# Kernel tuning notes

Hardware: AMD Instinct MI355X
Metric: run time of the kernel (lower is better)

The kernel has to match this reference:

```python
import jax, jax.numpy as jnp
import numpy as np

# config constants (init_kwargs)
WC, WS = 0.5, 0.5            # boundary cosine / structural weights (hybrid mode)
TARGET_BPP = 6.0             # target_bytes_per_patch
GAIN = 1.0                   # target_patch_gain
THRESH = 0.5                 # boundary_threshold; mask = p >= THRESH
EPS = 1e-6

_POP6 = jnp.array([bin(i).count('1') for i in range(64)], dtype=jnp.int32)

def _pop6(x):
    return _POP6[jnp.clip(x, 0, 63)]

def _logit(p):
    p = jnp.clip(p, EPS, 1.0 - EPS)
    return jnp.log(p) - jnp.log1p(-p)

def _next(x):  # shift-left by one, zero-padded at end (matches torch q_next pattern)
    return jnp.concatenate([x[1:], jnp.zeros((1,), x.dtype)])

def _hist(vals, mask, bins):
    idx = jnp.where(mask, vals, bins)  # invalid -> out of range, dropped
    return jnp.zeros((bins,), jnp.int32).at[idx].add(1, mode='drop')


def setup_inputs() -> dict:
    key = jax.random.key(0)
    ks = jax.random.split(key, 6)
    B, S = 4, 1048576
    return {
        'boundary_logprobs': jax.random.normal(ks[0], (B, S), jnp.float32),
        'states': jax.random.randint(ks[1], (B, S), 0, 4096, jnp.int32),
        'q_class': jax.random.randint(ks[2], (B, S), 0, 64, jnp.int32),
        'family': jax.random.randint(ks[3], (B, S), 0, 4, jnp.int32),
        'micro_ref': jax.random.randint(ks[4], (B, S), 0, 64, jnp.int32),
        'valid_mask': jax.random.randint(ks[5], (B, S), 0, 2, jnp.int32).astype(bool),
    }


def reference(boundary_logprobs, states, q_class, family, micro_ref, valid_mask):
    B, S = valid_mask.shape
    v = valid_mask.reshape(-1)
    st = states.reshape(-1).astype(jnp.int32)
    q = q_class.reshape(-1).astype(jnp.int32)
    fam = family.reshape(-1).astype(jnp.int32)
    mic = micro_ref.reshape(-1).astype(jnp.int32)

    # --- structural boundary probs ---
    omega12 = st & 0xFFF
    c6 = ((omega12 >> 6) ^ omega12) & 63          # chirality6
    d_chi = jnp.clip(_pop6(c6 ^ _next(c6)).astype(jnp.float32) / 6.0, 0.0, 1.0)
    d_q = _pop6((q & 63) ^ (_next(q) & 63)).astype(jnp.float32) / 6.0
    fx = (fam & 3) ^ (_next(fam) & 3)
    d_fam = (((fx & 1) != 0).astype(jnp.float32) + ((fx & 2) != 0).astype(jnp.float32)) / 2.0
    score = jnp.clip(0.5 * d_chi + 0.35 * d_q + 0.15 * d_fam, EPS, 1.0)
    structural = jnp.where(v, score, 0.0)

    # --- combine with cosine probs (hybrid mode) ---
    cosine = jnp.exp(jnp.minimum(boundary_logprobs.reshape(-1), 0.0))
    combined = (WC * cosine + WS * structural) / max(WC + WS, 1e-6)

    # --- target bytes-per-patch rate adjustment ---
    vf = v.astype(jnp.float32)
    vc = jnp.maximum(jnp.sum(vf), 1.0)
    cur = jnp.clip(jnp.sum(combined * vf) / vc, 1e-4, 1.0 - 1e-4)
    tgt = max(1e-4, min(1.0 - 1e-4, 1.0 / TARGET_BPP))
    shift = _logit(jnp.asarray(tgt, jnp.float32)) - _logit(cur)
    combined = jax.nn.sigmoid(_logit(combined) + GAIN * shift)
    combined = jnp.clip(combined, EPS, 1.0 - EPS)
    combined_logprobs = jnp.log(combined)
    bmask = combined_logprobs >= jnp.log(jnp.asarray(THRESH, jnp.float32))

    # --- histograms over effective (valid) positions ---
    shell = _pop6(c6)
    q_hist64 = _hist(q, v, 64)
    family_hist4 = _hist(fam, v, 4)
    micro_hist64 = _hist(mic, v, 64)
    shell_hist7 = _hist(shell, v, 7)
    wt_q = _pop6(q & 63)
    q_weight_hist7 = _hist(wt_q, v, 7)
    bits = ((q & 63)[:, None] >> jnp.arange(6)) & 1            # [n, 6]
    bit_excitation6 = jnp.sum(bits * v[:, None].astype(jnp.int32), axis=0)

    # --- patch lengths (vectorized run-length over valid bytes) ---
    bv = bmask & v
    pos = jnp.cumsum(v.astype(jnp.int32))                      # 1-indexed valid position
    bpos = jnp.where(bv, pos, 0)
    prev = jax.lax.cummax(jnp.concatenate([jnp.zeros((1,), jnp.int32), bpos[:-1]]))
    lengths = jnp.where(bv, pos - prev, 0)                     # dense run lengths at boundaries
    total_valid = pos[-1]
    trailing = total_valid - jax.lax.cummax(bpos)[-1]          # open trailing run
    patch_count = jnp.sum(bv).astype(jnp.int32) + (trailing > 0).astype(jnp.int32)

    return (combined_logprobs.reshape(B, S), bmask.reshape(B, S), structural.reshape(B, S),
            q_hist64, family_hist4, micro_hist64, shell_hist7, q_weight_hist7,
            bit_excitation6, lengths, trailing, patch_count)
```

## Files before the change

### kernel.cpp

```cpp
#include <hip/hip_runtime.h>

#define TPB 256
#define EPT 8
#define CHUNK (TPB * EPT)
#define P2T 1024
#define NSLICE 64

typedef unsigned long long ull;
typedef long long ll;

__device__ __forceinline__ ull shfl_down_u64(ull x, int off) {
    unsigned lo = (unsigned)x, hi = (unsigned)(x >> 32);
    lo = __shfl_down(lo, off, 64);
    hi = __shfl_down(hi, off, 64);
    return ((ull)hi << 32) | lo;
}

__global__ __launch_bounds__(TPB, 8) void k_pass1(
    const float* __restrict__ blp, const int* __restrict__ st,
    const int* __restrict__ q, const int* __restrict__ fam,
    const int* __restrict__ mic, const int* __restrict__ vm,
    float* __restrict__ out_structural,
    int* __restrict__ ghist, ull* __restrict__ l1sum, int n)
{
    __shared__ int lh2[2048];
    __shared__ int slhs[11];
    __shared__ int swv[4];
    __shared__ float swc[4];

    const int tid = threadIdx.x, lane = tid & 63, wave = tid >> 6;
    const long i0 = (long)blockIdx.x * CHUNK + (long)tid * EPT;
    const bool fast = ((long)(blockIdx.x + 1) * CHUNK <= n);

    int stv[9], qv[9], fv[9], micv[8], vmv[8];
    float bpv[8];
    if (fast) {
        const int4 sa = *(const int4*)(st + i0),  sb = *(const int4*)(st + i0 + 4);
        const int4 qa = *(const int4*)(q + i0),   qb = *(const int4*)(q + i0 + 4);
        const int4 fa = *(const int4*)(fam + i0), fb = *(const int4*)(fam + i0 + 4);
        const int4 ma = *(const int4*)(mic + i0), mb = *(const int4*)(mic + i0 + 4);
        const int4 va = *(const int4*)(vm + i0),  vb = *(const int4*)(vm + i0 + 4);
        const float4 ba = *(const float4*)(blp + i0), bb = *(const float4*)(blp + i0 + 4);
        int nst = __shfl_down(sa.x, 1, 64);
        int nq  = __shfl_down(qa.x, 1, 64);
        int nf  = __shfl_down(fa.x, 1, 64);
        if (lane == 63) {
            const long j = i0 + 8;
            nst = (j < n) ? st[j]  : 0;
            nq  = (j < n) ? q[j]   : 0;
            nf  = (j < n) ? fam[j] : 0;
        }
        stv[0]=sa.x; stv[1]=sa.y; stv[2]=sa.z; stv[3]=sa.w; stv[4]=sb.x; stv[5]=sb.y; stv[6]=sb.z; stv[7]=sb.w; stv[8]=nst;
        qv[0]=qa.x;  qv[1]=qa.y;  qv[2]=qa.z;  qv[3]=qa.w;  qv[4]=qb.x;  qv[5]=qb.y;  qv[6]=qb.z;  qv[7]=qb.w;  qv[8]=nq;
        fv[0]=fa.x;  fv[1]=fa.y;  fv[2]=fa.z;  fv[3]=fa.w;  fv[4]=fb.x;  fv[5]=fb.y;  fv[6]=fb.z;  fv[7]=fb.w;  fv[8]=nf;
        micv[0]=ma.x; micv[1]=ma.y; micv[2]=ma.z; micv[3]=ma.w; micv[4]=mb.x; micv[5]=mb.y; micv[6]=mb.z; micv[7]=mb.w;
        vmv[0]=va.x; vmv[1]=va.y; vmv[2]=va.z; vmv[3]=va.w; vmv[4]=vb.x; vmv[5]=vb.y; vmv[6]=vb.z; vmv[7]=vb.w;
        bpv[0]=ba.x; bpv[1]=ba.y; bpv[2]=ba.z; bpv[3]=ba.w; bpv[4]=bb.x; bpv[5]=bb.y; bpv[6]=bb.z; bpv[7]=bb.w;
    } else {
        #pragma unroll
        for (int e = 0; e < 8; ++e) {
            long ii = i0 + e;
            bool r = ii < n;
            stv[e] = r ? st[ii] : 0;  qv[e] = r ? q[ii] : 0;  fv[e] = r ? fam[ii] : 0;
            micv[e] = r ? mic[ii] : 0; vmv[e] = r ? vm[ii] : 0; bpv[e] = r ? blp[ii] : 0.f;
        }
        stv[8] = (i0 + 8 < n) ? st[i0 + 8] : 0;
        qv[8]  = (i0 + 8 < n) ? q[i0 + 8] : 0;
        fv[8]  = (i0 + 8 < n) ? fam[i0 + 8] : 0;
    }

    {
        int4 z4; z4.x = 0; z4.y = 0; z4.z = 0; z4.w = 0;
        *(int4*)&lh2[tid * 8] = z4;
        *(int4*)&lh2[tid * 8 + 4] = z4;
    }
    if (tid < 11) slhs[tid] = 0;
    __syncthreads();

    const int qrow = ((wave << 2) | (lane & 3)) << 6;
    int sv = 0;
    float scf = 0.0f;
    ull accF = 0, accS0 = 0, accS1 = 0;
    float structural[8];
    #pragma unroll
    for (int e = 0; e < 8; ++e) {
        int sti = stv[e], qi = qv[e], fi = fv[e], mi = micv[e];
        int v = (vmv[e] != 0);
        int om  = sti & 0xFFF;      int c6  = ((om  >> 6) ^ om ) & 63;
        int omn = stv[e+1] & 0xFFF; int c6n = ((omn >> 6) ^ omn) & 63;
        float d_chi = (float)__popc(c6 ^ c6n) * (1.0f / 6.0f);
        float d_q   = (float)__popc((qi & 63) ^ (qv[e+1] & 63)) * (1.0f / 6.0f);
        int fx = (fi & 3) ^ (fv[e+1] & 3);
        float d_fam = (float)((fx & 1) + ((fx >> 1) & 1)) * 0.5f;
        float score = 0.5f * d_chi + 0.35f * d_q + 0.15f * d_fam;
        score = fminf(fmaxf(score, 1e-6f), 1.0f);
        structural[e] = v ? score : 0.0f;
        float cosine = expf(fminf(bpv[e], 0.0f));
        float combined = 0.5f * (cosine + structural[e]);
        if (v) {
            sv += 1;
            scf += combined;
            atomicAdd(&lh2[qrow + (qi & 63)], 1);
            atomicAdd(&lh2[1024 + qrow + (mi & 63)], 1);
            accF += 1ULL << ((fi & 3) * 16);
            int sh = __popc(c6);
            ull ts = 1ULL << ((sh & 3) * 16);
            if (sh < 4) accS0 += ts; else accS1 += ts;
        }
    }

    if (fast) {
        float4 o;
        o.x=structural[0]; o.y=structural[1]; o.z=structural[2]; o.w=structural[3];
        *(float4*)(out_structural + i0) = o;
        o.x=structural[4]; o.y=structural[5]; o.z=structural[6]; o.w=structural[7];
        *(float4*)(out_structural + i0 + 4) = o;
    } else {
        #pragma unroll
        for (int e = 0; e < 8; ++e)
            if (i0 + e < n) out_structural[i0 + e] = structural[e];
    }

    #pragma unroll
    for (int off = 32; off > 0; off >>= 1) {
        sv  += __shfl_down(sv, off, 64);
        scf += __shfl_down(scf, off, 64);
        accF  += shfl_down_u64(accF, off);
        accS0 += shfl_down_u64(accS0, off);
        accS1 += shfl_down_u64(accS1, off);
    }
    if (lane == 0) {
        swv[wave] = sv; swc[wave] = scf;
        #pragma unroll
        for (int b2 = 0; b2 < 4; ++b2) atomicAdd(&slhs[b2],     (int)((accF  >> (16*b2)) & 0xFFFF));
        #pragma unroll
        for (int b2 = 0; b2 < 4; ++b2) atomicAdd(&slhs[4 + b2], (int)((accS0 >> (16*b2)) & 0xFFFF));
        #pragma unroll
        for (int b2 = 0; b2 < 3; ++b2) atomicAdd(&slhs[8 + b2], (int)((accS1 >> (16*b2)) & 0xFFFF));
    }
    __syncthreads();
    if (tid == 0) {
        int vsum = swv[0] + swv[1] + swv[2] + swv[3];
        double cs = (double)swc[0] + (double)swc[1] + (double)swc[2] + (double)swc[3];
        ll cf = (ll)(cs * 16384.0 + 0.5);
        atomicAdd(&l1sum[blockIdx.x >> 5], ((ull)(unsigned)vsum << 39) | (ull)cf);
    }
    if (tid < 139) {
        const int t2 = tid;
        int val;
        if (t2 < 64) {
            val = 0;
            #pragma unroll
            for (int r = 0; r < 16; ++r) val += lh2[(r << 6) + t2];
        } else if (t2 < 68) {
            val = slhs[t2 - 64];
        } else if (t2 < 132) {
            int b2 = t2 - 68;
            val = 0;
            #pragma unroll
            for (int r = 0; r < 16; ++r) val += lh2[1024 + (r << 6) + b2];
        } else {
            val = slhs[4 + (t2 - 132)];
        }
        if (val) atomicAdd(&ghist[(blockIdx.x & (NSLICE - 1)) * 152 + t2], val);
    }
}

__global__ __launch_bounds__(TPB, 8) void k_pass3(
    const float* __restrict__ strc, const float* __restrict__ blp,
    const ull* __restrict__ l1sum, const int* __restrict__ ghist,
    float* __restrict__ out_logp, float* __restrict__ out_bmask,
    float* __restrict__ out_len, int* __restrict__ chunk_cnt,
    int* __restrict__ chunk_lastloc, ull* __restrict__ chunk_first,
    int* __restrict__ chunk_vsum, float* __restrict__ out_hist, int n)
{
    __shared__ int swt[4], swm[4], scnt[4];
    __shared__ float sShift;
    __shared__ int qh[64];
    const int tid = threadIdx.x, lane = tid & 63, wave = tid >> 6;
    const long i0 = (long)blockIdx.x * CHUNK + (long)tid * EPT;
    const bool fast = ((long)(blockIdx.x + 1) * CHUNK <= n);
    const int nb = (int)gridDim.x;

    float sv8[8], bp8[8];
    if (fast) {
        const float4 s0 = *(const float4*)(strc + i0), s1 = *(const float4*)(strc + i0 + 4);
        const float4 p0 = *(const float4*)(blp + i0),  p1 = *(const float4*)(blp + i0 + 4);
        sv8[0]=s0.x; sv8[1]=s0.y; sv8[2]=s0.z; sv8[3]=s0.w; sv8[4]=s1.x; sv8[5]=s1.y; sv8[6]=s1.z; sv8[7]=s1.w;
        bp8[0]=p0.x; bp8[1]=p0.y; bp8[2]=p0.z; bp8[3]=p0.w; bp8[4]=p1.x; bp8[5]=p1.y; bp8[6]=p1.z; bp8[7]=p1.w;
    } else {
        #pragma unroll
        for (int e = 0; e < 8; ++e) {
            long ii = i0 + e;
            bool r = ii < n;
            sv8[e] = r ? strc[ii] : 0.0f;
            bp8[e] = r ? blp[ii] : 0.0f;
        }
    }

    if (wave == 0) {
        const int ngrp = (nb + 31) >> 5;
        int vt = 0; ll ct = 0;
        for (int gg = lane; gg < ngrp; gg += 64) {
            ull cell = l1sum[gg];
            vt += (int)(cell >> 39);
            ct += (ll)(cell & ((1ULL << 39) - 1));
        }
        #pragma unroll
        for (int off = 32; off > 0; off >>= 1) {
            vt += __shfl_down(vt, off, 64);
            ct += (ll)shfl_down_u64((ull)ct, off);
        }
        if (lane == 0) {
            double vcd = (double)(vt > 1 ? vt : 1);
            float cur = (float)(((double)ct * (1.0 / 16384.0)) / vcd);
            cur = fminf(fmaxf(cur, 1e-4f), 0.9999f);
            float p = fminf(fmaxf(cur, 1e-6f), 0.999999f);
            float lc = logf(p) - log1pf(-p);
            float tgt = (float)(1.0 / 6.0);
            float lt = logf(tgt) - log1pf(-tgt);
            sShift = lt - lc;
        }
    }
    __syncthreads();
    const float K = expf(-sShift);

    unsigned mv = 0, mb = 0;
    float lp[8], bmf[8], lenv[8];
    #pragma unroll
    for (int e = 0; e < 8; ++e) {
        float s = sv8[e];
        int v = (s > 0.0f);
        float cosine = expf(fminf(bp8[e], 0.0f));
        float comb = 0.5f * (cosine + s);
        float p = fminf(fmaxf(comb, 1e-6f), 0.999999f);
        float d = fmaf(K, 1.0f - p, p);
        float sgm = p / d;
        sgm = fminf(fmaxf(sgm, 1e-6f), 0.999999f);
        float clp = logf(sgm);
        lp[e] = clp;
        int bm = (clp >= -0.69314718f) ? 1 : 0;
        bmf[e] = (float)bm;
        mv |= (unsigned)v << e;
        if (bm & v) mb |= 1u << e;
        lenv[e] = 0.0f;
    }
    if (fast) {
        float4 o;
        o.x=lp[0]; o.y=lp[1]; o.z=lp[2]; o.w=lp[3];     *(float4*)(out_logp + i0) = o;
        o.x=lp[4]; o.y=lp[5]; o.z=lp[6]; o.w=lp[7];     *(float4*)(out_logp + i0 + 4) = o;
        o.x=bmf[0]; o.y=bmf[1]; o.z=bmf[2]; o.w=bmf[3]; *(float4*)(out_bmask + i0) = o;
        o.x=bmf[4]; o.y=bmf[5]; o.z=bmf[6]; o.w=bmf[7]; *(float4*)(out_bmask + i0 + 4) = o;
    } else {
        #pragma unroll
        for (int e = 0; e < 8; ++e)
            if (i0 + e < n) { out_logp[i0 + e] = lp[e]; out_bmask[i0 + e] = bmf[e]; }
    }

    int tvc = __popc(mv);
    int x = tvc;
    #pragma unroll
    for (int off = 1; off < 64; off <<= 1) {
        int y = __shfl_up(x, off, 64);
        if (lane >= off) x += y;
    }
    if (lane == 63) swt[wave] = x;
    __syncthreads();
    int wb = 0;
    for (int w2 = 0; w2 < wave; ++w2) wb += swt[w2];
    const int vbase = wb + (x - tvc);

    int last = -1;
    if (mb) {
        int hb = 31 - __clz(mb);
        last = vbase + __popc(mv & ((2u << hb) - 1));
    }
    int m = last;
    #pragma unroll
    for (int off = 1; off < 64; off <<= 1) {
        int y = __shfl_up(m, off, 64);
        if (lane >= off && y > m) m = y;
    }
    int exm = __shfl_up(m, 1, 64);
    if (lane == 0) exm = -1;
    if (lane == 63) swm[wave] = m;
    int cnt = __popc(mb);
    ull fp = ~0ULL;
    if (mb) {
        int lb = __ffs(mb) - 1;
        int fv2 = vbase + __popc(mv & ((2u << lb) - 1));
        fp = ((ull)(unsigned)(i0 + lb) << 32) | (unsigned)fv2;
    }
    #pragma unroll
    for (int off = 32; off > 0; off >>= 1) {
        cnt += __shfl_down(cnt, off, 64);
        ull fo = shfl_down_u64(fp, off);
        if (fo < fp) fp = fo;
    }
    __shared__ ull sfirst[4];
    if (lane == 0) { scnt[wave] = cnt; sfirst[wave] = fp; }
    __syncthreads();

    int prev = exm;
    for (int w2 = 0; w2 < wave; ++w2) if (swm[w2] > prev) prev = swm[w2];
    int runv = 0;
    #pragma unroll
    for (int e = 0; e < 8; ++e) {
        runv += (mv >> e) & 1;
        if ((mb >> e) & 1) {
            int pos = vbase + runv;
            lenv[e] = (prev >= 0) ? (float)(pos - prev) : 0.0f;
            prev = pos;
        }
    }
    if (fast) {
        float4 o;
        o.x=lenv[0]; o.y=lenv[1]; o.z=lenv[2]; o.w=lenv[3]; *(float4*)(out_len + i0) = o;
        o.x=lenv[4]; o.y=lenv[5]; o.z=lenv[6]; o.w=lenv[7]; *(float4*)(out_len + i0 + 4) = o;
    } else {
        #pragma unroll
        for (int e = 0; e < 8; ++e)
            if (i0 + e < n) out_len[i0 + e] = lenv[e];
    }
    if (tid == 0) {
        int c = scnt[0] + scnt[1] + scnt[2] + scnt[3];
        int L = swm[0];
        if (swm[1] > L) L = swm[1];
        if (swm[2] > L) L = swm[2];
        if (swm[3] > L) L = swm[3];
        ull F = sfirst[0];
        if (sfirst[1] < F) F = sfirst[1];
        if (sfirst[2] < F) F = sfirst[2];
        if (sfirst[3] < F) F = sfirst[3];
        chunk_cnt[blockIdx.x] = c;
        chunk_lastloc[blockIdx.x] = L > 0 ? L : 0;
        chunk_first[blockIdx.x] = F;
        chunk_vsum[blockIdx.x] = swt[0] + swt[1] + swt[2] + swt[3];
    }

    if (blockIdx.x == 0) {
        if (tid < 139) {
            int acc = 0;
            #pragma unroll 8
            for (int sl = 0; sl < NSLICE; ++sl) acc += ghist[sl * 152 + tid];
            out_hist[tid] = (float)acc;
            if (tid < 64) qh[tid] = acc;
        }
        __syncthreads();
        if (tid < 7) {
            int sacc = 0;
            for (int b = 0; b < 64; ++b) if (__popc(b) == tid) sacc += qh[b];
            out_hist[139 + tid] = (float)sacc;
        }
        if (tid < 6) {
            int sacc = 0;
            for (int b = 0; b < 64; ++b) sacc += qh[b] * ((b >> tid) & 1);
            out_hist[146 + tid] = (float)sacc;
        }
    }
}

__global__ __launch_bounds__(P2T) void k_pass4(
    const int* __restrict__ chunk_cnt, const int* __restrict__ chunk_lastloc,
    const ull* __restrict__ chunk_first, const int* __restrict__ chunk_vsum,
    int nb, float* __restrict__ out_len,
    float* __restrict__ out_trailing, float* __restrict__ out_patch)
{
    __shared__ int ss[P2T];
    __shared__ int sm[P2T];
    __shared__ int sc[P2T];
    int t = threadIdx.x;
    int c0 = 2 * t, c1 = 2 * t + 1;
    int v0 = (c0 < nb) ? chunk_vsum[c0] : 0;
    int v1 = (c1 < nb) ? chunk_vsum[c1] : 0;
    int l0 = (c0 < nb) ? chunk_lastloc[c0] : 0;
    int l1 = (c1 < nb) ? chunk_lastloc[c1] : 0;
    int k0 = (c0 < nb) ? chunk_cnt[c0] : 0;
    int k1 = (c1 < nb) ? chunk_cnt[c1] : 0;
    ss[t] = v0 + v1;
    sc[t] = k0 + k1;
    __syncthreads();
    for (int off = 1; off < P2T; off <<= 1) {
        int add = (t >= off) ? ss[t - off] : 0;
        __syncthreads();
        ss[t] += add;
        __syncthreads();
    }
    const int vbase0 = ss[t] - v0 - v1;
    const int vbase1 = ss[t] - v1;
    const int total_v = ss[P2T - 1];
    const int gl0 = (l0 > 0) ? vbase0 + l0 : 0;
    const int gl1 = (l1 > 0) ? vbase1 + l1 : 0;
    sm[t] = gl0 > gl1 ? gl0 : gl1;
    __syncthreads();
    for (int off = 1; off < P2T; off <<= 1) {
        int y = (t >= off) ? sm[t - off] : 0;
        __syncthreads();
        if (y > sm[t]) sm[t] = y;
        __syncthreads();
    }
    const int excl = (t > 0) ? sm[t - 1] : 0;
    if (c0 < nb) {
        ull F = chunk_first[c0];
        if (F != ~0ULL) {
            int fi = (int)(F >> 32);
            int fv = (int)(F & 0xFFFFFFFFu);
            out_len[fi] = (float)(vbase0 + fv - excl);
        }
    }
    const int carry1 = excl > gl0 ? excl : gl0;
    if (c1 < nb) {
        ull F = chunk_first[c1];
        if (F != ~0ULL) {
            int fi = (int)(F >> 32);
            int fv = (int)(F & 0xFFFFFFFFu);
            out_len[fi] = (float)(vbase1 + fv - carry1);
        }
    }
    const int gmax = sm[P2T - 1];
    __syncthreads();
    for (int off = P2T / 2; off > 0; off >>= 1) {
        if (t < off) sc[t] += sc[t + off];
        __syncthreads();
    }
    if (t == 0) {
        int trailing = total_v - gmax;
        *out_trailing = (float)trailing;
        *out_patch = (float)(sc[0] + (trailing > 0 ? 1 : 0));
    }
}

extern "C" void kernel_launch(void* const* d_in, const int* in_sizes, int n_in,
                              void* d_out, int out_size, void* d_ws, size_t ws_size,
                              hipStream_t stream)
{
    const float* blp = (const float*)d_in[0];
    const int* st   = (const int*)d_in[1];
    const int* q    = (const int*)d_in[2];
    const int* fam  = (const int*)d_in[3];
    const int* mic  = (const int*)d_in[4];
    const int* vm   = (const int*)d_in[5];
    const int n = in_sizes[0];
    const int nb = (n + CHUNK - 1) / CHUNK;

    float* out = (float*)d_out;
    float* out_logp       = out;
    float* out_bmask      = out + (size_t)n;
    float* out_structural = out + 2 * (size_t)n;
    float* out_hist       = out + 3 * (size_t)n;
    float* out_len        = out + 3 * (size_t)n + 152;
    float* out_trailing   = out + 4 * (size_t)n + 152;
    float* out_patch      = out + 4 * (size_t)n + 153;

    char* w = (char*)d_ws;
    int*  ghist         = (int*)(w);
    ull*  l1sum         = (ull*)(w + 38912);
    int*  chunk_cnt     = (int*)(w + 40960);
    int*  chunk_lastloc = (int*)(w + 49152);
    int*  chunk_vsum    = (int*)(w + 57344);
    ull*  chunk_first   = (ull*)(w + 65536);

    hipMemsetAsync(w, 0, 39424, stream);

    k_pass1<<<dim3(nb), dim3(TPB), 0, stream>>>(
        blp, st, q, fam, mic, vm, out_structural, ghist, l1sum, n);

    k_pass3<<<dim3(nb), dim3(TPB), 0, stream>>>(
        out_structural, blp, l1sum, ghist,
        out_logp, out_bmask, out_len, chunk_cnt, chunk_lastloc, chunk_first,
        chunk_vsum, out_hist, n);

    k_pass4<<<dim3(1), dim3(P2T), 0, stream>>>(
        chunk_cnt, chunk_lastloc, chunk_first, chunk_vsum, nb, out_len,
        out_trailing, out_patch);
}
```

Measured before the change: 173.4 us.

## Halve elements per thread and scan four chunks per thread in pass4

Cuts elements per thread from 8 to 4, doubling the block count of pass1 and pass3 to raise parallelism and spread the per-block atomics and reductions. With N=4M this gives 4096 chunks, so the single-block pass4 scan now has each thread handle four chunks serially. The workspace offsets and memset size grow to fit the larger per-chunk arrays. The trade-off is more blocks doing block-level setup, more global histogram atomics, and a longer serial section in pass4.

```diff
diff --git a/kernel.cpp b/kernel.cpp
--- a/kernel.cpp
+++ b/kernel.cpp
@@ -1,7 +1,7 @@
 #include <hip/hip_runtime.h>
 
 #define TPB 256
-#define EPT 8
+#define EPT 4
 #define CHUNK (TPB * EPT)
 #define P2T 1024
 #define NSLICE 64
@@ -32,41 +32,41 @@
     const long i0 = (long)blockIdx.x * CHUNK + (long)tid * EPT;
     const bool fast = ((long)(blockIdx.x + 1) * CHUNK <= n);
 
-    int stv[9], qv[9], fv[9], micv[8], vmv[8];
-    float bpv[8];
+    int stv[5], qv[5], fv[5], micv[4], vmv[4];
+    float bpv[4];
     if (fast) {
-        const int4 sa = *(const int4*)(st + i0),  sb = *(const int4*)(st + i0 + 4);
-        const int4 qa = *(const int4*)(q + i0),   qb = *(const int4*)(q + i0 + 4);
-        const int4 fa = *(const int4*)(fam + i0), fb = *(const int4*)(fam + i0 + 4);
-        const int4 ma = *(const int4*)(mic + i0), mb = *(const int4*)(mic + i0 + 4);
-        const int4 va = *(const int4*)(vm + i0),  vb = *(const int4*)(vm + i0 + 4);
-        const float4 ba = *(const float4*)(blp + i0), bb = *(const float4*)(blp + i0 + 4);
+        const int4 sa = *(const int4*)(st + i0);
+        const int4 qa = *(const int4*)(q + i0);
+        const int4 fa = *(const int4*)(fam + i0);
+        const int4 ma = *(const int4*)(mic + i0);
+        const int4 va = *(const int4*)(vm + i0);
+        const float4 ba = *(const float4*)(blp + i0);
         int nst = __shfl_down(sa.x, 1, 64);
         int nq  = __shfl_down(qa.x, 1, 64);
         int nf  = __shfl_down(fa.x, 1, 64);
         if (lane == 63) {
-            const long j = i0 + 8;
+            const long j = i0 + 4;
             nst = (j < n) ? st[j]  : 0;
             nq  = (j < n) ? q[j]   : 0;
             nf  = (j < n) ? fam[j] : 0;
         }
-        stv[0]=sa.x; stv[1]=sa.y; stv[2]=sa.z; stv[3]=sa.w; stv[4]=sb.x; stv[5]=sb.y; stv[6]=sb.z; stv[7]=sb.w; stv[8]=nst;
-        qv[0]=qa.x;  qv[1]=qa.y;  qv[2]=qa.z;  qv[3]=qa.w;  qv[4]=qb.x;  qv[5]=qb.y;  qv[6]=qb.z;  qv[7]=qb.w;  qv[8]=nq;
-        fv[0]=fa.x;  fv[1]=fa.y;  fv[2]=fa.z;  fv[3]=fa.w;  fv[4]=fb.x;  fv[5]=fb.y;  fv[6]=fb.z;  fv[7]=fb.w;  fv[8]=nf;
-        micv[0]=ma.x; micv[1]=ma.y; micv[2]=ma.z; micv[3]=ma.w; micv[4]=mb.x; micv[5]=mb.y; micv[6]=mb.z; micv[7]=mb.w;
-        vmv[0]=va.x; vmv[1]=va.y; vmv[2]=va.z; vmv[3]=va.w; vmv[4]=vb.x; vmv[5]=vb.y; vmv[6]=vb.z; vmv[7]=vb.w;
-        bpv[0]=ba.x; bpv[1]=ba.y; bpv[2]=ba.z; bpv[3]=ba.w; bpv[4]=bb.x; bpv[5]=bb.y; bpv[6]=bb.z; bpv[7]=bb.w;
+        stv[0]=sa.x; stv[1]=sa.y; stv[2]=sa.z; stv[3]=sa.w; stv[4]=nst;
+        qv[0]=qa.x;  qv[1]=qa.y;  qv[2]=qa.z;  qv[3]=qa.w;  qv[4]=nq;
+        fv[0]=fa.x;  fv[1]=fa.y;  fv[2]=fa.z;  fv[3]=fa.w;  fv[4]=nf;
+        micv[0]=ma.x; micv[1]=ma.y; micv[2]=ma.z; micv[3]=ma.w;
+        vmv[0]=va.x; vmv[1]=va.y; vmv[2]=va.z; vmv[3]=va.w;
+        bpv[0]=ba.x; bpv[1]=ba.y; bpv[2]=ba.z; bpv[3]=ba.w;
     } else {
         #pragma unroll
-        for (int e = 0; e < 8; ++e) {
+        for (int e = 0; e < 4; ++e) {
             long ii = i0 + e;
             bool r = ii < n;
             stv[e] = r ? st[ii] : 0;  qv[e] = r ? q[ii] : 0;  fv[e] = r ? fam[ii] : 0;
             micv[e] = r ? mic[ii] : 0; vmv[e] = r ? vm[ii] : 0; bpv[e] = r ? blp[ii] : 0.f;
         }
-        stv[8] = (i0 + 8 < n) ? st[i0 + 8] : 0;
-        qv[8]  = (i0 + 8 < n) ? q[i0 + 8] : 0;
-        fv[8]  = (i0 + 8 < n) ? fam[i0 + 8] : 0;
+        stv[4] = (i0 + 4 < n) ? st[i0 + 4] : 0;
+        qv[4]  = (i0 + 4 < n) ? q[i0 + 4] : 0;
+        fv[4]  = (i0 + 4 < n) ? fam[i0 + 4] : 0;
     }
 
     {
@@ -81,9 +81,9 @@
     int sv = 0;
     float scf = 0.0f;
     ull accF = 0, accS0 = 0, accS1 = 0;
-    float structural[8];
-    #pragma unroll
-    for (int e = 0; e < 8; ++e) {
+    float structural[4];
+    #pragma unroll
+    for (int e = 0; e < 4; ++e) {
         int sti = stv[e], qi = qv[e], fi = fv[e], mi = micv[e];
         int v = (vmv[e] != 0);
         int om  = sti & 0xFFF;      int c6  = ((om  >> 6) ^ om ) & 63;
@@ -113,11 +113,9 @@
         float4 o;
         o.x=structural[0]; o.y=structural[1]; o.z=structural[2]; o.w=structural[3];
         *(float4*)(out_structural + i0) = o;
-        o.x=structural[4]; o.y=structural[5]; o.z=structural[6]; o.w=structural[7];
-        *(float4*)(out_structural + i0 + 4) = o;
     } else {
         #pragma unroll
-        for (int e = 0; e < 8; ++e)
+        for (int e = 0; e < 4; ++e)
             if (i0 + e < n) out_structural[i0 + e] = structural[e];
     }
 
@@ -175,6 +173,7 @@
     int* __restrict__ chunk_vsum, float* __restrict__ out_hist, int n)
 {
     __shared__ int swt[4], swm[4], scnt[4];
+    __shared__ ull sfirst[4];
     __shared__ float sShift;
     __shared__ int qh[64];
     const int tid = threadIdx.x, lane = tid & 63, wave = tid >> 6;
@@ -182,19 +181,19 @@
     const bool fast = ((long)(blockIdx.x + 1) * CHUNK <= n);
     const int nb = (int)gridDim.x;
 
-    float sv8[8], bp8[8];
+    float sv4[4], bp4[4];
     if (fast) {
-        const float4 s0 = *(const float4*)(strc + i0), s1 = *(const float4*)(strc + i0 + 4);
-        const float4 p0 = *(const float4*)(blp + i0),  p1 = *(const float4*)(blp + i0 + 4);
-        sv8[0]=s0.x; sv8[1]=s0.y; sv8[2]=s0.z; sv8[3]=s0.w; sv8[4]=s1.x; sv8[5]=s1.y; sv8[6]=s1.z; sv8[7]=s1.w;
-        bp8[0]=p0.x; bp8[1]=p0.y; bp8[2]=p0.z; bp8[3]=p0.w; bp8[4]=p1.x; bp8[5]=p1.y; bp8[6]=p1.z; bp8[7]=p1.w;
+        const float4 s0 = *(const float4*)(strc + i0);
+        const float4 p0 = *(const float4*)(blp + i0);
+        sv4[0]=s0.x; sv4[1]=s0.y; sv4[2]=s0.z; sv4[3]=s0.w;
+        bp4[0]=p0.x; bp4[1]=p0.y; bp4[2]=p0.z; bp4[3]=p0.w;
     } else {
         #pragma unroll
-        for (int e = 0; e < 8; ++e) {
+        for (int e = 0; e < 4; ++e) {
             long ii = i0 + e;
             bool r = ii < n;
-            sv8[e] = r ? strc[ii] : 0.0f;
-            bp8[e] = r ? blp[ii] : 0.0f;
+            sv4[e] = r ? strc[ii] : 0.0f;
+            bp4[e] = r ? blp[ii] : 0.0f;
         }
     }
 
@@ -226,12 +225,12 @@
     const float K = expf(-sShift);
 
     unsigned mv = 0, mb = 0;
-    float lp[8], bmf[8], lenv[8];
-    #pragma unroll
-    for (int e = 0; e < 8; ++e) {
-        float s = sv8[e];
+    float lp[4], bmf[4], lenv[4];
+    #pragma unroll
+    for (int e = 0; e < 4; ++e) {
+        float s = sv4[e];
         int v = (s > 0.0f);
-        float cosine = expf(fminf(bp8[e], 0.0f));
+        float cosine = expf(fminf(bp4[e], 0.0f));
         float comb = 0.5f * (cosine + s);
         float p = fminf(fmaxf(comb, 1e-6f), 0.999999f);
         float d = fmaf(K, 1.0f - p, p);
@@ -248,12 +247,10 @@
     if (fast) {
         float4 o;
         o.x=lp[0]; o.y=lp[1]; o.z=lp[2]; o.w=lp[3];     *(float4*)(out_logp + i0) = o;
-        o.x=lp[4]; o.y=lp[5]; o.z=lp[6]; o.w=lp[7];     *(float4*)(out_logp + i0 + 4) = o;
         o.x=bmf[0]; o.y=bmf[1]; o.z=bmf[2]; o.w=bmf[3]; *(float4*)(out_bmask + i0) = o;
-        o.x=bmf[4]; o.y=bmf[5]; o.z=bmf[6]; o.w=bmf[7]; *(float4*)(out_bmask + i0 + 4) = o;
     } else {
         #pragma unroll
-        for (int e = 0; e < 8; ++e)
+        for (int e = 0; e < 4; ++e)
             if (i0 + e < n) { out_logp[i0 + e] = lp[e]; out_bmask[i0 + e] = bmf[e]; }
     }
 
@@ -297,7 +294,6 @@
         ull fo = shfl_down_u64(fp, off);
         if (fo < fp) fp = fo;
     }
-    __shared__ ull sfirst[4];
     if (lane == 0) { scnt[wave] = cnt; sfirst[wave] = fp; }
     __syncthreads();
 
@@ -305,7 +301,7 @@
     for (int w2 = 0; w2 < wave; ++w2) if (swm[w2] > prev) prev = swm[w2];
     int runv = 0;
     #pragma unroll
-    for (int e = 0; e < 8; ++e) {
+    for (int e = 0; e < 4; ++e) {
         runv += (mv >> e) & 1;
         if ((mb >> e) & 1) {
             int pos = vbase + runv;
@@ -316,10 +312,9 @@
     if (fast) {
         float4 o;
         o.x=lenv[0]; o.y=lenv[1]; o.z=lenv[2]; o.w=lenv[3]; *(float4*)(out_len + i0) = o;
-        o.x=lenv[4]; o.y=lenv[5]; o.z=lenv[6]; o.w=lenv[7]; *(float4*)(out_len + i0 + 4) = o;
     } else {
         #pragma unroll
-        for (int e = 0; e < 8; ++e)
+        for (int e = 0; e < 4; ++e)
             if (i0 + e < n) out_len[i0 + e] = lenv[e];
     }
     if (tid == 0) {
@@ -369,16 +364,23 @@
     __shared__ int ss[P2T];
     __shared__ int sm[P2T];
     __shared__ int sc[P2T];
-    int t = threadIdx.x;
-    int c0 = 2 * t, c1 = 2 * t + 1;
-    int v0 = (c0 < nb) ? chunk_vsum[c0] : 0;
-    int v1 = (c1 < nb) ? chunk_vsum[c1] : 0;
-    int l0 = (c0 < nb) ? chunk_lastloc[c0] : 0;
-    int l1 = (c1 < nb) ? chunk_lastloc[c1] : 0;
-    int k0 = (c0 < nb) ? chunk_cnt[c0] : 0;
-    int k1 = (c1 < nb) ? chunk_cnt[c1] : 0;
-    ss[t] = v0 + v1;
-    sc[t] = k0 + k1;
+    const int t = threadIdx.x;
+    int v[4], l[4]; ull F[4];
+    int vpre[4];
+    int vs = 0, ks = 0, rmax = 0;
+    #pragma unroll
+    for (int e = 0; e < 4; ++e) {
+        int c = t * 4 + e;
+        vpre[e] = vs;
+        v[e] = (c < nb) ? chunk_vsum[c] : 0;
+        l[e] = (c < nb) ? chunk_lastloc[c] : 0;
+        int k = (c < nb) ? chunk_cnt[c] : 0;
+        F[e] = (c < nb) ? chunk_first[c] : ~0ULL;
+        if (l[e] > 0) { int gl = vs + l[e]; if (gl > rmax) rmax = gl; }
+        vs += v[e];
+        ks += k;
+    }
+    ss[t] = vs; sc[t] = ks;
     __syncthreads();
     for (int off = 1; off < P2T; off <<= 1) {
         int add = (t >= off) ? ss[t - off] : 0;
@@ -386,12 +388,9 @@
         ss[t] += add;
         __syncthreads();
     }
-    const int vbase0 = ss[t] - v0 - v1;
-    const int vbase1 = ss[t] - v1;
+    const int base = ss[t] - vs;
     const int total_v = ss[P2T - 1];
-    const int gl0 = (l0 > 0) ? vbase0 + l0 : 0;
-    const int gl1 = (l1 > 0) ? vbase1 + l1 : 0;
-    sm[t] = gl0 > gl1 ? gl0 : gl1;
+    sm[t] = (rmax > 0) ? base + rmax : 0;
     __syncthreads();
     for (int off = 1; off < P2T; off <<= 1) {
         int y = (t >= off) ? sm[t - off] : 0;
@@ -399,25 +398,18 @@
         if (y > sm[t]) sm[t] = y;
         __syncthreads();
     }
-    const int excl = (t > 0) ? sm[t - 1] : 0;
-    if (c0 < nb) {
-        ull F = chunk_first[c0];
-        if (F != ~0ULL) {
-            int fi = (int)(F >> 32);
-            int fv = (int)(F & 0xFFFFFFFFu);
-            out_len[fi] = (float)(vbase0 + fv - excl);
-        }
-    }
-    const int carry1 = excl > gl0 ? excl : gl0;
-    if (c1 < nb) {
-        ull F = chunk_first[c1];
-        if (F != ~0ULL) {
-            int fi = (int)(F >> 32);
-            int fv = (int)(F & 0xFFFFFFFFu);
-            out_len[fi] = (float)(vbase1 + fv - carry1);
-        }
-    }
+    int scarry = (t > 0) ? sm[t - 1] : 0;
     const int gmax = sm[P2T - 1];
+    #pragma unroll
+    for (int e = 0; e < 4; ++e) {
+        if (F[e] != ~0ULL) {
+            int fi = (int)(F[e] >> 32);
+            int fv = (int)(F[e] & 0xFFFFFFFFu);
+            out_len[fi] = (float)(base + vpre[e] + fv - scarry);
+        }
+        int gl = (l[e] > 0) ? base + vpre[e] + l[e] : 0;
+        if (gl > scarry) scarry = gl;
+    }
     __syncthreads();
     for (int off = P2T / 2; off > 0; off >>= 1) {
         if (t < off) sc[t] += sc[t + off];
@@ -456,11 +448,11 @@
     int*  ghist         = (int*)(w);
     ull*  l1sum         = (ull*)(w + 38912);
     int*  chunk_cnt     = (int*)(w + 40960);
-    int*  chunk_lastloc = (int*)(w + 49152);
-    int*  chunk_vsum    = (int*)(w + 57344);
-    ull*  chunk_first   = (ull*)(w + 65536);
-
-    hipMemsetAsync(w, 0, 39424, stream);
+    int*  chunk_lastloc = (int*)(w + 57344);
+    int*  chunk_vsum    = (int*)(w + 73728);
+    ull*  chunk_first   = (ull*)(w + 90112);
+
+    hipMemsetAsync(w, 0, 39936, stream);
 
     k_pass1<<<dim3(nb), dim3(TPB), 0, stream>>>(
         blp, st, q, fam, mic, vm, out_structural, ghist, l1sum, n);
```

After: 181.7 us. +4.8%, slower.
